# Kernel optimization log

Hardware: AMD Instinct MI355X
Metric: run time of the kernel (lower is better)

The kernel has to match this reference:

```python
import jax, jax.numpy as jnp
import numpy as np

H, E, K = 1024, 8, 2  # hidden_size, num_experts, top_k
B, S = 2, 4096


def setup_inputs() -> dict:
    key = jax.random.key(0)
    ks = jax.random.split(key, 5)
    s = 1.0 / np.sqrt(H)
    return {
        "x": jax.random.normal(ks[0], (B, S, H), dtype=jnp.float32),
        "ln_scale": jnp.ones((H,), jnp.float32),
        "ln_bias": jnp.zeros((H,), jnp.float32),
        "w1": (jax.random.normal(ks[1], (H, H), jnp.float32) * s),
        "b1": jnp.zeros((H,), jnp.float32),
        "w2": (jax.random.normal(ks[2], (H, E), jnp.float32) * s),
        "b2": jnp.zeros((E,), jnp.float32),
        "We": (jax.random.normal(ks[3], (E, H, H), jnp.float32) * s),
        "be": jnp.zeros((E, H), jnp.float32),
    }


def _layernorm(x, scale, bias, eps=1e-5):
    m = jnp.mean(x, axis=-1, keepdims=True)
    v = jnp.var(x, axis=-1, keepdims=True)
    return (x - m) * jax.lax.rsqrt(v + eps) * scale + bias


def reference(x, ln_scale, ln_bias, w1, b1, w2, b2, We, be):
    b, s, h = x.shape
    # --- router (BaseRouter): LN -> MLP -> softmax -> top-k -> renorm ---
    xn = _layernorm(x, ln_scale, ln_bias)
    hmid = jax.nn.relu(xn @ w1 + b1)
    logits = hmid @ w2 + b2                      # [B,S,E]
    probs = jax.nn.softmax(logits, axis=-1)
    topk_p, topk_i = jax.lax.top_k(probs, K)     # [B,S,K]
    topk_p = topk_p / jnp.sum(topk_p, axis=-1, keepdims=True)
    # sparse combine weights [B,S,E]: renormalized top-k gate, 0 elsewhere
    cw = jnp.sum(topk_p[..., None] * jax.nn.one_hot(topk_i, E, dtype=x.dtype), axis=-2)
    # --- expert dispatch / weighted combine ---
    t = b * s
    xf = x.reshape(t, h)
    cwf = cw.reshape(t, E)
    ye = jnp.einsum('th,ehd->etd', xf, We) + be[:, None, :]   # [E,T,H]
    out = jnp.einsum('te,etd->td', cwf, ye).reshape(b, s, h)
    # --- aux load-balance loss ---
    mean_p = jnp.mean(probs, axis=(0, 1))        # [E]
    aux = jnp.sum(mean_p * jnp.log(mean_p * E + 1e-9))
    return out, aux
```

## Files before the change

### kernel.cpp

```cpp
#include <hip/hip_runtime.h>
#include <hip/hip_fp16.h>

#define H 1024
#define E 8
#define TT 8192

typedef __attribute__((ext_vector_type(8))) short bf16x8;
typedef __attribute__((ext_vector_type(4))) float f32x4;

__device__ __forceinline__ unsigned short f2bf(float f) {
  unsigned int u = __float_as_uint(f);
  u += 0x7fffu + ((u >> 16) & 1u);
  return (unsigned short)(u >> 16);
}

__device__ __forceinline__ int swz(int row, int c) {
  return (row << 5) | (((c ^ (row >> 1)) & 3) << 3);
}

__device__ __forceinline__ void gld16(void* lds, const void* g) {
  __builtin_amdgcn_global_load_lds((const __attribute__((address_space(1))) void*)g,
                                   (__attribute__((address_space(3))) void*)lds, 16, 0, 0);
}

__global__ __launch_bounds__(64) void k_init(int* cnt, double* psum) {
  int t = threadIdx.x;
  if (t < E) { cnt[t] = 0; psum[t] = 0.0; }
}

__global__ __launch_bounds__(256) void k_cast_we(const float* __restrict__ we, unsigned short* __restrict__ wet) {
  __shared__ unsigned short tile[32][33];
  int e = blockIdx.z;
  int kb = blockIdx.x << 5, nb = blockIdx.y << 5;
  int t = threadIdx.x;
  int cc = t & 31, rr = t >> 5;
  size_t base = (size_t)e * H * H;
#pragma unroll
  for (int r = 0; r < 4; ++r) {
    int k = kb + rr + (r << 3);
    tile[rr + (r << 3)][cc] = f2bf(we[base + (size_t)k * H + nb + cc]);
  }
  __syncthreads();
#pragma unroll
  for (int r = 0; r < 4; ++r) {
    int n = nb + rr + (r << 3);
    wet[base + (size_t)n * H + kb + cc] = tile[cc][rr + (r << 3)];
  }
}

__global__ __launch_bounds__(256) void k_cast_w1(const float* __restrict__ w1, const float* __restrict__ lsc,
                                                 unsigned short* __restrict__ w1h, unsigned short* __restrict__ w1l) {
  __shared__ float tile[32][33];
  int kb = blockIdx.x << 5, nb = blockIdx.y << 5;
  int t = threadIdx.x;
  int cc = t & 31, rr = t >> 5;
#pragma unroll
  for (int r = 0; r < 4; ++r) {
    int k = kb + rr + (r << 3);
    tile[rr + (r << 3)][cc] = w1[(size_t)k * H + nb + cc] * lsc[k];
  }
  __syncthreads();
#pragma unroll
  for (int r = 0; r < 4; ++r) {
    int n = nb + rr + (r << 3);
    float v = tile[cc][rr + (r << 3)];
    unsigned short h = f2bf(v);
    float hv = __uint_as_float((unsigned)h << 16);
    unsigned short l = f2bf(v - hv);
    w1h[(size_t)n * H + kb + cc] = h;
    w1l[(size_t)n * H + kb + cc] = l;
  }
}

__global__ __launch_bounds__(256) void k_b1a(const float* __restrict__ w1, const float* __restrict__ lbi,
                                             float* __restrict__ part) {
  int bk = blockIdx.x, t = threadIdx.x;
  float a0 = 0, a1 = 0, a2 = 0, a3 = 0;
  for (int kk = 0; kk < 16; ++kk) {
    int k = (bk << 4) + kk;
    float lb = lbi[k];
    const float* row = &w1[(size_t)k * H];
    a0 = fmaf(lb, row[t], a0);
    a1 = fmaf(lb, row[t + 256], a1);
    a2 = fmaf(lb, row[t + 512], a2);
    a3 = fmaf(lb, row[t + 768], a3);
  }
  part[bk * H + t] = a0;
  part[bk * H + t + 256] = a1;
  part[bk * H + t + 512] = a2;
  part[bk * H + t + 768] = a3;
}

__global__ __launch_bounds__(256) void k_b1b(const float* __restrict__ part, const float* __restrict__ b1,
                                             float* __restrict__ b1eff) {
  int n = (blockIdx.x << 8) + threadIdx.x;
  float s = b1[n];
  for (int j = 0; j < 64; ++j) s += part[j * H + n];
  b1eff[n] = s;
}

__global__ __launch_bounds__(256) void k_stats(const float* __restrict__ x, float2* __restrict__ stats,
                                               unsigned short* __restrict__ xb) {
  int tok = blockIdx.x, t = threadIdx.x;
  const float4 v = *reinterpret_cast<const float4*>(&x[(size_t)tok * H + (t << 2)]);
  float s = v.x + v.y + v.z + v.w;
  float ss = v.x * v.x + v.y * v.y + v.z * v.z + v.w * v.w;
#pragma unroll
  for (int off = 32; off; off >>= 1) { s += __shfl_down(s, off); ss += __shfl_down(ss, off); }
  __shared__ float red[4][2];
  int lane = t & 63, wv = t >> 6;
  if (lane == 0) { red[wv][0] = s; red[wv][1] = ss; }
  __syncthreads();
  float fs = red[0][0] + red[1][0] + red[2][0] + red[3][0];
  float fss = red[0][1] + red[1][1] + red[2][1] + red[3][1];
  float mean = fs * (1.0f / H);
  float var = fss * (1.0f / H) - mean * mean;
  float rstd = rsqrtf(var + 1e-5f);
  if (t == 0) stats[tok] = make_float2(mean, rstd);
  ushort4 ob;
  ob.x = f2bf(v.x); ob.y = f2bf(v.y); ob.z = f2bf(v.z); ob.w = f2bf(v.w);
  *reinterpret_cast<ushort4*>(&xb[(size_t)tok * H + (t << 2)]) = ob;
}

__global__ __launch_bounds__(256) void k_router_mfma(
    const float* __restrict__ x, const float2* __restrict__ stats,
    const unsigned short* __restrict__ w1h, const unsigned short* __restrict__ w1l,
    const float* __restrict__ b1eff, const float* __restrict__ w2, float* __restrict__ plog) {
  __shared__ __align__(16) short At[2][8192];
  __shared__ __align__(16) short Bt[2][8192];
  int t = threadIdx.x;
  int d = blockIdx.x + (blockIdx.y << 6);
  int l = ((d & 7) << 6) + (d >> 3);
  int bm = (l & 63) << 7, bnb = l >> 6, bn = bnb << 7;
  int w = t >> 6, lane = t & 63;
  int s0 = (w << 8) + lane;
  int r0_ = s0 >> 2, cg0 = (s0 & 3) ^ ((r0_ >> 1) & 3);
  int s1 = s0 + 64, r1_ = s1 >> 2, cg1 = (s1 & 3) ^ ((r1_ >> 1) & 3);
  int s2 = s0 + 128, r2_ = s2 >> 2, cg2 = (s2 & 3) ^ ((r2_ >> 1) & 3);
  int s3 = s0 + 192, r3_ = s3 >> 2, cg3 = (s3 & 3) ^ ((r3_ >> 1) & 3);
  const unsigned short* srcB0 =
      ((r0_ < 128) ? &w1h[(size_t)(bn + r0_) * H] : &w1l[(size_t)(bn + r0_ - 128) * H]) + (cg0 << 3);
  const unsigned short* srcB1 =
      ((r1_ < 128) ? &w1h[(size_t)(bn + r1_) * H] : &w1l[(size_t)(bn + r1_ - 128) * H]) + (cg1 << 3);
  const unsigned short* srcB2 =
      ((r2_ < 128) ? &w1h[(size_t)(bn + r2_) * H] : &w1l[(size_t)(bn + r2_ - 128) * H]) + (cg2 << 3);
  const unsigned short* srcB3 =
      ((r3_ < 128) ? &w1h[(size_t)(bn + r3_) * H] : &w1l[(size_t)(bn + r3_ - 128) * H]) + (cg3 << 3);
  int dB0 = (w << 11), dB1 = dB0 + 512, dB2 = dB0 + 1024, dB3 = dB0 + 1536;
  int arow = t >> 1, ac0 = (t & 1) << 1;
  float2 mr = stats[bm + arow];
  float rsc = mr.y, mb = -mr.x * mr.y;
  const float* xsrc = &x[(size_t)(bm + arow) * H + (ac0 << 3)];
  int wA0 = swz(arow, ac0), wA1 = swz(arow, ac0 + 1);
  int wL0 = swz(arow + 128, ac0), wL1 = swz(arow + 128, ac0 + 1);
  float4 va0, va1, va2, va3;
  auto ldx = [&](int ko) {
    va0 = *(const float4*)(xsrc + ko + 0); va1 = *(const float4*)(xsrc + ko + 4);
    va2 = *(const float4*)(xsrc + ko + 8); va3 = *(const float4*)(xsrc + ko + 12);
  };
  auto stageB = [&](int b, int ko) {
    gld16(&Bt[b][dB0], srcB0 + ko); gld16(&Bt[b][dB1], srcB1 + ko);
    gld16(&Bt[b][dB2], srcB2 + ko); gld16(&Bt[b][dB3], srcB3 + ko);
  };
  auto split_store = [&](int b) {
    float zz[16];
    zz[0] = fmaf(va0.x, rsc, mb); zz[1] = fmaf(va0.y, rsc, mb);
    zz[2] = fmaf(va0.z, rsc, mb); zz[3] = fmaf(va0.w, rsc, mb);
    zz[4] = fmaf(va1.x, rsc, mb); zz[5] = fmaf(va1.y, rsc, mb);
    zz[6] = fmaf(va1.z, rsc, mb); zz[7] = fmaf(va1.w, rsc, mb);
    zz[8] = fmaf(va2.x, rsc, mb); zz[9] = fmaf(va2.y, rsc, mb);
    zz[10] = fmaf(va2.z, rsc, mb); zz[11] = fmaf(va2.w, rsc, mb);
    zz[12] = fmaf(va3.x, rsc, mb); zz[13] = fmaf(va3.y, rsc, mb);
    zz[14] = fmaf(va3.z, rsc, mb); zz[15] = fmaf(va3.w, rsc, mb);
    unsigned hw[8], lw[8];
#pragma unroll
    for (int p = 0; p < 8; ++p) {
      unsigned ua = __float_as_uint(zz[2 * p]), ub = __float_as_uint(zz[2 * p + 1]);
      hw[p] = (ua >> 16) | (ub & 0xffff0000u);
      float la = zz[2 * p] - __uint_as_float(ua & 0xffff0000u);
      float lb = zz[2 * p + 1] - __uint_as_float(ub & 0xffff0000u);
      lw[p] = (__float_as_uint(la) >> 16) | (__float_as_uint(lb) & 0xffff0000u);
    }
    *(int4*)&At[b][wA0] = make_int4(hw[0], hw[1], hw[2], hw[3]);
    *(int4*)&At[b][wA1] = make_int4(hw[4], hw[5], hw[6], hw[7]);
    *(int4*)&At[b][wL0] = make_int4(lw[0], lw[1], lw[2], lw[3]);
    *(int4*)&At[b][wL1] = make_int4(lw[4], lw[5], lw[6], lw[7]);
  };
  int wr = (w >> 1) << 6, wc = (w & 1) << 6;
  int l15 = lane & 15, lgp = lane >> 4;
  f32x4 acc[4][4];
#pragma unroll
  for (int i = 0; i < 4; ++i)
#pragma unroll
    for (int j = 0; j < 4; ++j) acc[i][j] = f32x4{0.f, 0.f, 0.f, 0.f};
  ldx(0);
  stageB(0, 0);
  split_store(0);
  for (int kt = 0; kt < 32; ++kt) {
    int b = kt & 1;
    if (kt < 31) {
      ldx((kt + 1) << 5);
      stageB(b ^ 1, (kt + 1) << 5);
    }
    if (kt < 31) {
      asm volatile("s_waitcnt vmcnt(8) lgkmcnt(0)" ::: "memory");
    } else {
      asm volatile("s_waitcnt vmcnt(0) lgkmcnt(0)" ::: "memory");
    }
    __builtin_amdgcn_s_barrier();
    bf16x8 bh[4], bl[4];
#pragma unroll
    for (int j = 0; j < 4; ++j) {
      bh[j] = *(const bf16x8*)&Bt[b][swz(wc + (j << 4) + l15, lgp)];
      bl[j] = *(const bf16x8*)&Bt[b][swz(128 + wc + (j << 4) + l15, lgp)];
    }
#pragma unroll
    for (int i = 0; i < 4; ++i) {
      bf16x8 ah = *(const bf16x8*)&At[b][swz(wr + (i << 4) + l15, lgp)];
      bf16x8 al = *(const bf16x8*)&At[b][swz(128 + wr + (i << 4) + l15, lgp)];
#pragma unroll
      for (int j = 0; j < 4; ++j) {
        acc[i][j] = __builtin_amdgcn_mfma_f32_16x16x32_bf16(ah, bh[j], acc[i][j], 0, 0, 0);
        acc[i][j] = __builtin_amdgcn_mfma_f32_16x16x32_bf16(ah, bl[j], acc[i][j], 0, 0, 0);
        acc[i][j] = __builtin_amdgcn_mfma_f32_16x16x32_bf16(al, bh[j], acc[i][j], 0, 0, 0);
      }
    }
    if (kt < 31) {
      split_store(b ^ 1);
      asm volatile("s_waitcnt lgkmcnt(0)" ::: "memory");
      __builtin_amdgcn_s_barrier();
    }
  }
  float w2r[4][8], b1r[4];
#pragma unroll
  for (int j = 0; j < 4; ++j) {
    int col = bn + wc + (j << 4) + l15;
    float4 p0 = *(const float4*)&w2[(size_t)col * E];
    float4 p1 = *(const float4*)&w2[(size_t)col * E + 4];
    w2r[j][0] = p0.x; w2r[j][1] = p0.y; w2r[j][2] = p0.z; w2r[j][3] = p0.w;
    w2r[j][4] = p1.x; w2r[j][5] = p1.y; w2r[j][6] = p1.z; w2r[j][7] = p1.w;
    b1r[j] = b1eff[col];
  }
#pragma unroll
  for (int i = 0; i < 4; ++i)
#pragma unroll
    for (int j = 0; j < 4; ++j)
#pragma unroll
      for (int r = 0; r < 4; ++r) acc[i][j][r] = fmaxf(acc[i][j][r] + b1r[j], 0.f);
  int wh = wc >> 6;
  size_t pbase = ((size_t)(bnb * 2 + wh) * TT + bm) * E;
#pragma unroll
  for (int e = 0; e < E; ++e) {
    float se[4][4];
#pragma unroll
    for (int i = 0; i < 4; ++i)
#pragma unroll
      for (int r = 0; r < 4; ++r)
        se[i][r] = acc[i][0][r] * w2r[0][e] + acc[i][1][r] * w2r[1][e] +
                   acc[i][2][r] * w2r[2][e] + acc[i][3][r] * w2r[3][e];
#pragma unroll
    for (int off = 1; off < 16; off <<= 1)
#pragma unroll
      for (int i = 0; i < 4; ++i)
#pragma unroll
        for (int r = 0; r < 4; ++r) se[i][r] += __shfl_xor(se[i][r], off);
    if (l15 == 0) {
#pragma unroll
      for (int i = 0; i < 4; ++i)
#pragma unroll
        for (int r = 0; r < 4; ++r) {
          int row = wr + (i << 4) + (lgp << 2) + r;
          plog[pbase + (size_t)row * E + e] = se[i][r];
        }
    }
  }
}

__global__ __launch_bounds__(256) void k_top(const float* __restrict__ plog, const float* __restrict__ b2,
                                             int* __restrict__ topE, float* __restrict__ topW,
                                             int* __restrict__ listIdx, float* __restrict__ listW,
                                             int* __restrict__ cnt, double* __restrict__ psum) {
  int t = threadIdx.x, lane = t & 63;
  int tok = (blockIdx.x << 8) + t;
  float lg[E], p[E];
  float4 ba = *reinterpret_cast<const float4*>(b2);
  float4 bb = *reinterpret_cast<const float4*>(b2 + 4);
  lg[0] = ba.x; lg[1] = ba.y; lg[2] = ba.z; lg[3] = ba.w;
  lg[4] = bb.x; lg[5] = bb.y; lg[6] = bb.z; lg[7] = bb.w;
#pragma unroll
  for (int nb = 0; nb < 16; ++nb) {
    const float* pp = &plog[((size_t)nb * TT + tok) * E];
    float4 q0 = *reinterpret_cast<const float4*>(pp);
    float4 q1 = *reinterpret_cast<const float4*>(pp + 4);
    lg[0] += q0.x; lg[1] += q0.y; lg[2] += q0.z; lg[3] += q0.w;
    lg[4] += q1.x; lg[5] += q1.y; lg[6] += q1.z; lg[7] += q1.w;
  }
  float m = lg[0];
#pragma unroll
  for (int e = 1; e < E; ++e) m = fmaxf(m, lg[e]);
  float s = 0.f;
#pragma unroll
  for (int e = 0; e < E; ++e) { p[e] = __expf(lg[e] - m); s += p[e]; }
  float inv = 1.f / s;
#pragma unroll
  for (int e = 0; e < E; ++e) p[e] *= inv;
  {
    float ps[E];
#pragma unroll
    for (int e = 0; e < E; ++e) ps[e] = p[e];
#pragma unroll
    for (int off = 1; off < 64; off <<= 1)
#pragma unroll
      for (int e = 0; e < E; ++e) ps[e] += __shfl_xor(ps[e], off);
    if (lane == 0)
#pragma unroll
      for (int e = 0; e < E; ++e) atomicAdd(&psum[e], (double)ps[e]);
  }
  int e0 = 0;
#pragma unroll
  for (int e = 1; e < E; ++e) if (p[e] > p[e0]) e0 = e;
  int e1 = (e0 == 0) ? 1 : 0;
#pragma unroll
  for (int e = 0; e < E; ++e) if (e != e0 && p[e] > p[e1]) e1 = e;
  float rsw = 1.f / (p[e0] + p[e1]);
  float w0 = p[e0] * rsw, w1v = p[e1] * rsw;
  topE[tok << 1] = e0; topE[(tok << 1) + 1] = e1;
  topW[tok << 1] = w0; topW[(tok << 1) + 1] = w1v;
  unsigned long long lt = (1ull << lane) - 1ull;
#pragma unroll
  for (int e = 0; e < E; ++e) {
    unsigned long long m0 = __ballot(e0 == e);
    unsigned long long m1 = __ballot(e1 == e);
    int n0 = __popcll(m0), total = n0 + __popcll(m1);
    if (total == 0) continue;
    int leader = __ffsll(m0 | m1) - 1;
    int base = 0;
    if (lane == leader) base = atomicAdd(&cnt[e], total);
    base = __shfl(base, leader);
    if (e0 == e) {
      int pos = e * TT + base + __popcll(m0 & lt);
      listIdx[pos] = (tok << 1); listW[pos] = w0;
    }
    if (e1 == e) {
      int pos = e * TT + base + n0 + __popcll(m1 & lt);
      listIdx[pos] = (tok << 1) | 1; listW[pos] = w1v;
    }
  }
}

__global__ __launch_bounds__(256) void k_expert_gemm(const unsigned short* __restrict__ xb,
                                                     const unsigned short* __restrict__ wet,
                                                     const int* __restrict__ listIdx, const float* __restrict__ listW,
                                                     const int* __restrict__ cnt, unsigned short* __restrict__ ys) {
  int d = blockIdx.x + (blockIdx.y << 6) + (blockIdx.z << 9);
  int l = ((d & 7) << 9) + (d >> 3);
  int e = l >> 9, by = (l >> 6) & 7, bx = l & 63;
  int c = cnt[e];
  int r0 = bx << 7;
  if (r0 >= c) return;
  int n0 = by << 7;
  __shared__ __align__(16) short A[3][4096], B[3][4096];
  __shared__ int gi[128];
  __shared__ float gw[128];
  int t = threadIdx.x;
  if (t < 128) {
    int rr = r0 + t;
    gi[t] = (rr < c) ? listIdx[e * TT + rr] : -1;
    gw[t] = (rr < c) ? listW[e * TT + rr] : 0.f;
  }
  __syncthreads();
  int w = t >> 6, lane = t & 63;
  int s0 = (w << 7) + lane, s1 = s0 + 64;
  int rA0 = s0 >> 2, cg0 = (s0 & 3) ^ ((rA0 >> 1) & 3);
  int rA1 = s1 >> 2, cg1 = (s1 & 3) ^ ((rA1 >> 1) & 3);
  int pk0 = gi[rA0], pk1 = gi[rA1];
  const unsigned short* srcA0 = &xb[(size_t)((pk0 < 0) ? 0 : (pk0 >> 1)) * H + (cg0 << 3)];
  const unsigned short* srcA1 = &xb[(size_t)((pk1 < 0) ? 0 : (pk1 >> 1)) * H + (cg1 << 3)];
  size_t wbase = (size_t)e * H * H;
  const unsigned short* srcB0 = &wet[wbase + (size_t)(n0 + rA0) * H + (cg0 << 3)];
  const unsigned short* srcB1 = &wet[wbase + (size_t)(n0 + rA1) * H + (cg1 << 3)];
  int d0 = (w << 10), d1 = d0 + 512;
  int wr = (w >> 1) << 6, wc = (w & 1) << 6;
  int l15 = lane & 15, lgp = lane >> 4;
  f32x4 acc[4][4];
#pragma unroll
  for (int i = 0; i < 4; ++i)
#pragma unroll
    for (int j = 0; j < 4; ++j) acc[i][j] = f32x4{0.f, 0.f, 0.f, 0.f};
#pragma unroll
  for (int pt = 0; pt < 3; ++pt) {
    int ko = pt << 5;
    gld16(&A[pt][d0], srcA0 + ko); gld16(&A[pt][d1], srcA1 + ko);
    gld16(&B[pt][d0], srcB0 + ko); gld16(&B[pt][d1], srcB1 + ko);
  }
  int b = 0;
  for (int kt = 0; kt < 32; ++kt) {
    if (kt <= 29) {
      asm volatile("s_waitcnt vmcnt(8)" ::: "memory");
    } else if (kt == 30) {
      asm volatile("s_waitcnt vmcnt(4)" ::: "memory");
    } else {
      asm volatile("s_waitcnt vmcnt(0)" ::: "memory");
    }
    __builtin_amdgcn_s_barrier();
    bf16x8 bq[4];
#pragma unroll
    for (int j = 0; j < 4; ++j) bq[j] = *(const bf16x8*)&B[b][swz(wc + (j << 4) + l15, lgp)];
#pragma unroll
    for (int i = 0; i < 4; ++i) {
      bf16x8 af = *(const bf16x8*)&A[b][swz(wr + (i << 4) + l15, lgp)];
#pragma unroll
      for (int j = 0; j < 4; ++j)
        acc[i][j] = __builtin_amdgcn_mfma_f32_16x16x32_bf16(af, bq[j], acc[i][j], 0, 0, 0);
    }
    if (kt < 29) {
      __builtin_amdgcn_s_barrier();
      int ko = (kt + 3) << 5;
      gld16(&A[b][d0], srcA0 + ko); gld16(&A[b][d1], srcA1 + ko);
      gld16(&B[b][d0], srcB0 + ko); gld16(&B[b][d1], srcB1 + ko);
    }
    b = (b == 2) ? 0 : b + 1;
  }
#pragma unroll
  for (int i = 0; i < 4; ++i) {
#pragma unroll
    for (int r = 0; r < 4; ++r) {
      int row = wr + (i << 4) + (lgp << 2) + r;
      int pk = gi[row];
      if (pk < 0) continue;
      int tok = pk >> 1, slot = pk & 1;
      float wgt = gw[row];
      size_t ob = ((size_t)slot * TT + tok) * H + n0 + wc + l15;
#pragma unroll
      for (int j = 0; j < 4; ++j) ys[ob + (j << 4)] = __half_as_ushort(__float2half(wgt * acc[i][j][r]));
    }
  }
}

__global__ __launch_bounds__(256) void k_combine(const unsigned short* __restrict__ ys, const int* __restrict__ topE,
                                                 const float* __restrict__ topW, const float* __restrict__ be,
                                                 float* __restrict__ out) {
  int tok = blockIdx.x, t = threadIdx.x;
  int e0 = topE[tok << 1], e1 = topE[(tok << 1) + 1];
  float w0 = topW[tok << 1], w1v = topW[(tok << 1) + 1];
  int h = t << 2;
  size_t base = (size_t)tok * H + h;
  ushort4 a = *reinterpret_cast<const ushort4*>(&ys[base]);
  ushort4 b = *reinterpret_cast<const ushort4*>(&ys[(size_t)TT * H + base]);
  float4 b0 = *reinterpret_cast<const float4*>(&be[e0 * H + h]);
  float4 b1v = *reinterpret_cast<const float4*>(&be[e1 * H + h]);
  float4 o;
  o.x = __half2float(__ushort_as_half(a.x)) + __half2float(__ushort_as_half(b.x)) + w0 * b0.x + w1v * b1v.x;
  o.y = __half2float(__ushort_as_half(a.y)) + __half2float(__ushort_as_half(b.y)) + w0 * b0.y + w1v * b1v.y;
  o.z = __half2float(__ushort_as_half(a.z)) + __half2float(__ushort_as_half(b.z)) + w0 * b0.z + w1v * b1v.z;
  o.w = __half2float(__ushort_as_half(a.w)) + __half2float(__ushort_as_half(b.w)) + w0 * b0.w + w1v * b1v.w;
  *reinterpret_cast<float4*>(&out[base]) = o;
}

__global__ __launch_bounds__(64) void k_aux(const double* __restrict__ psum, float* __restrict__ outAux) {
  if (threadIdx.x == 0) {
    double a = 0.0;
    for (int e = 0; e < E; ++e) {
      double mp = psum[e] / (double)TT;
      a += mp * log(mp * (double)E + 1e-9);
    }
    outAux[0] = (float)a;
  }
}

extern "C" void kernel_launch(void* const* d_in, const int* in_sizes, int n_in, void* d_out, int out_size, void* d_ws,
                              size_t ws_size, hipStream_t stream) {
  const float* x = (const float*)d_in[0];
  const float* lsc = (const float*)d_in[1];
  const float* lbi = (const float*)d_in[2];
  const float* w1 = (const float*)d_in[3];
  const float* b1 = (const float*)d_in[4];
  const float* w2 = (const float*)d_in[5];
  const float* b2 = (const float*)d_in[6];
  const float* we = (const float*)d_in[7];
  const float* be = (const float*)d_in[8];
  float* out = (float*)d_out;
  char* ws = (char*)d_ws;

  char* p = ws;
  float2* stats = (float2*)p; p += TT * 8;
  int* topE = (int*)p; p += TT * 2 * 4;
  float* topW = (float*)p; p += TT * 2 * 4;
  int* listIdx = (int*)p; p += E * TT * 4;
  float* listW = (float*)p; p += E * TT * 4;
  int* cnt = (int*)p; p += 256;
  double* psum = (double*)p; p += 2048;
  float* b1eff = (float*)p; p += H * 4;
  float* part = (float*)p; p += 64 * H * 4;
  unsigned short* xb = (unsigned short*)(ws + (2u << 20));
  unsigned short* wet = (unsigned short*)(ws + (18u << 20));
  unsigned short* w1h = (unsigned short*)(ws + (34u << 20));
  unsigned short* w1l = (unsigned short*)(ws + (36u << 20));
  float* plog = (float*)(ws + (38u << 20));
  unsigned short* ys = (unsigned short*)(ws + (34u << 20));

  k_init<<<1, 64, 0, stream>>>(cnt, psum);
  k_cast_w1<<<dim3(32, 32), 256, 0, stream>>>(w1, lsc, w1h, w1l);
  k_b1a<<<64, 256, 0, stream>>>(w1, lbi, part);
  k_b1b<<<4, 256, 0, stream>>>(part, b1, b1eff);
  k_cast_we<<<dim3(32, 32, E), 256, 0, stream>>>(we, wet);
  k_stats<<<TT, 256, 0, stream>>>(x, stats, xb);
  k_router_mfma<<<dim3(TT / 128, H / 128), 256, 0, stream>>>(x, stats, w1h, w1l, b1eff, w2, plog);
  k_top<<<TT / 256, 256, 0, stream>>>(plog, b2, topE, topW, listIdx, listW, cnt, psum);
  k_expert_gemm<<<dim3(TT / 128, H / 128, E), 256, 0, stream>>>(xb, wet, listIdx, listW, cnt, ys);
  k_combine<<<TT, 256, 0, stream>>>(ys, topE, topW, be, out);
  k_aux<<<1, 64, 0, stream>>>(psum, out + (size_t)TT * H);
}
```

Baseline: 250.5 us.

## Precompute split LN activations and load GEMM A-operands directly into registers

k_stats now writes the normalized activations as hi/lo bf16 arrays, so the router GEMM no longer reloads fp32 x and does the LN and split inside its K loop. Both the router and expert GEMMs now read their A fragments straight from global memory into registers with double buffering, and only B goes through a 3-stage LDS ring, which removes the A staging in LDS and one barrier per iteration. The grids are flattened to 1D with a remapped tile order, and the workspace is relaid so the expert-weight cast runs after the router. The cost is 32 MB of extra zh/zl global traffic and uncoalesced per-lane A loads, some of them gathered rows, that go straight to registers.

```diff
diff --git a/kernel.cpp b/kernel.cpp
--- a/kernel.cpp
+++ b/kernel.cpp
@@ -99,8 +99,8 @@
   b1eff[n] = s;
 }
 
-__global__ __launch_bounds__(256) void k_stats(const float* __restrict__ x, float2* __restrict__ stats,
-                                               unsigned short* __restrict__ xb) {
+__global__ __launch_bounds__(256) void k_stats(const float* __restrict__ x, unsigned short* __restrict__ xb,
+                                               unsigned short* __restrict__ zh, unsigned short* __restrict__ zl) {
   int tok = blockIdx.x, t = threadIdx.x;
   const float4 v = *reinterpret_cast<const float4*>(&x[(size_t)tok * H + (t << 2)]);
   float s = v.x + v.y + v.z + v.w;
@@ -116,119 +116,104 @@
   float mean = fs * (1.0f / H);
   float var = fss * (1.0f / H) - mean * mean;
   float rstd = rsqrtf(var + 1e-5f);
-  if (t == 0) stats[tok] = make_float2(mean, rstd);
+  float mb = -mean * rstd;
+  size_t base = (size_t)tok * H + (t << 2);
   ushort4 ob;
   ob.x = f2bf(v.x); ob.y = f2bf(v.y); ob.z = f2bf(v.z); ob.w = f2bf(v.w);
-  *reinterpret_cast<ushort4*>(&xb[(size_t)tok * H + (t << 2)]) = ob;
+  *reinterpret_cast<ushort4*>(&xb[base]) = ob;
+  float zz[4];
+  zz[0] = fmaf(v.x, rstd, mb); zz[1] = fmaf(v.y, rstd, mb);
+  zz[2] = fmaf(v.z, rstd, mb); zz[3] = fmaf(v.w, rstd, mb);
+  ushort4 oh, ol;
+  unsigned u0 = __float_as_uint(zz[0]), u1 = __float_as_uint(zz[1]);
+  unsigned u2 = __float_as_uint(zz[2]), u3 = __float_as_uint(zz[3]);
+  oh.x = (unsigned short)(u0 >> 16); oh.y = (unsigned short)(u1 >> 16);
+  oh.z = (unsigned short)(u2 >> 16); oh.w = (unsigned short)(u3 >> 16);
+  float l0 = zz[0] - __uint_as_float(u0 & 0xffff0000u);
+  float l1 = zz[1] - __uint_as_float(u1 & 0xffff0000u);
+  float l2 = zz[2] - __uint_as_float(u2 & 0xffff0000u);
+  float l3 = zz[3] - __uint_as_float(u3 & 0xffff0000u);
+  ol.x = (unsigned short)(__float_as_uint(l0) >> 16); ol.y = (unsigned short)(__float_as_uint(l1) >> 16);
+  ol.z = (unsigned short)(__float_as_uint(l2) >> 16); ol.w = (unsigned short)(__float_as_uint(l3) >> 16);
+  *reinterpret_cast<ushort4*>(&zh[base]) = oh;
+  *reinterpret_cast<ushort4*>(&zl[base]) = ol;
 }
 
 __global__ __launch_bounds__(256) void k_router_mfma(
-    const float* __restrict__ x, const float2* __restrict__ stats,
-    const unsigned short* __restrict__ w1h, const unsigned short* __restrict__ w1l,
+    const unsigned short* __restrict__ zh, const unsigned short* __restrict__ zl,
+    const unsigned short* __restrict__ w1h,
     const float* __restrict__ b1eff, const float* __restrict__ w2, float* __restrict__ plog) {
-  __shared__ __align__(16) short At[2][8192];
-  __shared__ __align__(16) short Bt[2][8192];
+  __shared__ __align__(16) short Bt[3][8192];
   int t = threadIdx.x;
-  int d = blockIdx.x + (blockIdx.y << 6);
+  int d = blockIdx.x;
   int l = ((d & 7) << 6) + (d >> 3);
-  int bm = (l & 63) << 7, bnb = l >> 6, bn = bnb << 7;
+  int bm = (l >> 3) << 7;
+  int bnb = l & 7, bn = bnb << 7;
   int w = t >> 6, lane = t & 63;
-  int s0 = (w << 8) + lane;
-  int r0_ = s0 >> 2, cg0 = (s0 & 3) ^ ((r0_ >> 1) & 3);
-  int s1 = s0 + 64, r1_ = s1 >> 2, cg1 = (s1 & 3) ^ ((r1_ >> 1) & 3);
-  int s2 = s0 + 128, r2_ = s2 >> 2, cg2 = (s2 & 3) ^ ((r2_ >> 1) & 3);
-  int s3 = s0 + 192, r3_ = s3 >> 2, cg3 = (s3 & 3) ^ ((r3_ >> 1) & 3);
-  const unsigned short* srcB0 =
-      ((r0_ < 128) ? &w1h[(size_t)(bn + r0_) * H] : &w1l[(size_t)(bn + r0_ - 128) * H]) + (cg0 << 3);
-  const unsigned short* srcB1 =
-      ((r1_ < 128) ? &w1h[(size_t)(bn + r1_) * H] : &w1l[(size_t)(bn + r1_ - 128) * H]) + (cg1 << 3);
-  const unsigned short* srcB2 =
-      ((r2_ < 128) ? &w1h[(size_t)(bn + r2_) * H] : &w1l[(size_t)(bn + r2_ - 128) * H]) + (cg2 << 3);
-  const unsigned short* srcB3 =
-      ((r3_ < 128) ? &w1h[(size_t)(bn + r3_) * H] : &w1l[(size_t)(bn + r3_ - 128) * H]) + (cg3 << 3);
-  int dB0 = (w << 11), dB1 = dB0 + 512, dB2 = dB0 + 1024, dB3 = dB0 + 1536;
-  int arow = t >> 1, ac0 = (t & 1) << 1;
-  float2 mr = stats[bm + arow];
-  float rsc = mr.y, mb = -mr.x * mr.y;
-  const float* xsrc = &x[(size_t)(bm + arow) * H + (ac0 << 3)];
-  int wA0 = swz(arow, ac0), wA1 = swz(arow, ac0 + 1);
-  int wL0 = swz(arow + 128, ac0), wL1 = swz(arow + 128, ac0 + 1);
-  float4 va0, va1, va2, va3;
-  auto ldx = [&](int ko) {
-    va0 = *(const float4*)(xsrc + ko + 0); va1 = *(const float4*)(xsrc + ko + 4);
-    va2 = *(const float4*)(xsrc + ko + 8); va3 = *(const float4*)(xsrc + ko + 12);
-  };
-  auto stageB = [&](int b, int ko) {
-    gld16(&Bt[b][dB0], srcB0 + ko); gld16(&Bt[b][dB1], srcB1 + ko);
-    gld16(&Bt[b][dB2], srcB2 + ko); gld16(&Bt[b][dB3], srcB3 + ko);
-  };
-  auto split_store = [&](int b) {
-    float zz[16];
-    zz[0] = fmaf(va0.x, rsc, mb); zz[1] = fmaf(va0.y, rsc, mb);
-    zz[2] = fmaf(va0.z, rsc, mb); zz[3] = fmaf(va0.w, rsc, mb);
-    zz[4] = fmaf(va1.x, rsc, mb); zz[5] = fmaf(va1.y, rsc, mb);
-    zz[6] = fmaf(va1.z, rsc, mb); zz[7] = fmaf(va1.w, rsc, mb);
-    zz[8] = fmaf(va2.x, rsc, mb); zz[9] = fmaf(va2.y, rsc, mb);
-    zz[10] = fmaf(va2.z, rsc, mb); zz[11] = fmaf(va2.w, rsc, mb);
-    zz[12] = fmaf(va3.x, rsc, mb); zz[13] = fmaf(va3.y, rsc, mb);
-    zz[14] = fmaf(va3.z, rsc, mb); zz[15] = fmaf(va3.w, rsc, mb);
-    unsigned hw[8], lw[8];
-#pragma unroll
-    for (int p = 0; p < 8; ++p) {
-      unsigned ua = __float_as_uint(zz[2 * p]), ub = __float_as_uint(zz[2 * p + 1]);
-      hw[p] = (ua >> 16) | (ub & 0xffff0000u);
-      float la = zz[2 * p] - __uint_as_float(ua & 0xffff0000u);
-      float lb = zz[2 * p + 1] - __uint_as_float(ub & 0xffff0000u);
-      lw[p] = (__float_as_uint(la) >> 16) | (__float_as_uint(lb) & 0xffff0000u);
-    }
-    *(int4*)&At[b][wA0] = make_int4(hw[0], hw[1], hw[2], hw[3]);
-    *(int4*)&At[b][wA1] = make_int4(hw[4], hw[5], hw[6], hw[7]);
-    *(int4*)&At[b][wL0] = make_int4(lw[0], lw[1], lw[2], lw[3]);
-    *(int4*)&At[b][wL1] = make_int4(lw[4], lw[5], lw[6], lw[7]);
-  };
+  int l15 = lane & 15, lgp = lane >> 4;
   int wr = (w >> 1) << 6, wc = (w & 1) << 6;
-  int l15 = lane & 15, lgp = lane >> 4;
+  int sl = (w << 8) + lane;
+  int bo[4];
+#pragma unroll
+  for (int q = 0; q < 4; ++q) {
+    int s = sl + (q << 6);
+    int r = s >> 2, cg = (s & 3) ^ ((r >> 1) & 3);
+    bo[q] = ((r < 128) ? (bn + r) * H : 1048576 + (bn + r - 128) * H) + (cg << 3);
+  }
+  int dB = w << 11;
+  int zo[4];
+#pragma unroll
+  for (int i = 0; i < 4; ++i) zo[i] = (bm + wr + (i << 4) + l15) * H + (lgp << 3);
   f32x4 acc[4][4];
 #pragma unroll
   for (int i = 0; i < 4; ++i)
 #pragma unroll
     for (int j = 0; j < 4; ++j) acc[i][j] = f32x4{0.f, 0.f, 0.f, 0.f};
-  ldx(0);
-  stageB(0, 0);
-  split_store(0);
+  bf16x8 ah[2][4], al[2][4];
+#pragma unroll
+  for (int q = 0; q < 4; ++q) gld16(&Bt[0][dB + (q << 9)], w1h + bo[q]);
+#pragma unroll
+  for (int q = 0; q < 4; ++q) gld16(&Bt[1][dB + (q << 9)], w1h + bo[q] + 32);
+#pragma unroll
+  for (int i = 0; i < 4; ++i) {
+    ah[0][i] = *(const bf16x8*)(zh + zo[i]);
+    al[0][i] = *(const bf16x8*)(zl + zo[i]);
+  }
+#pragma unroll
   for (int kt = 0; kt < 32; ++kt) {
-    int b = kt & 1;
+    const int cur = kt & 1, nxt = cur ^ 1;
     if (kt < 31) {
-      ldx((kt + 1) << 5);
-      stageB(b ^ 1, (kt + 1) << 5);
-    }
-    if (kt < 31) {
-      asm volatile("s_waitcnt vmcnt(8) lgkmcnt(0)" ::: "memory");
+      const int ko = (kt + 1) << 5;
+#pragma unroll
+      for (int i = 0; i < 4; ++i) {
+        ah[nxt][i] = *(const bf16x8*)(zh + zo[i] + ko);
+        al[nxt][i] = *(const bf16x8*)(zl + zo[i] + ko);
+      }
+    }
+    if (kt <= 30) {
+      asm volatile("s_waitcnt vmcnt(12)" ::: "memory");
     } else {
-      asm volatile("s_waitcnt vmcnt(0) lgkmcnt(0)" ::: "memory");
-    }
+      asm volatile("s_waitcnt vmcnt(0)" ::: "memory");
+    }
+    __builtin_amdgcn_sched_barrier(0);
     __builtin_amdgcn_s_barrier();
-    bf16x8 bh[4], bl[4];
+    __builtin_amdgcn_sched_barrier(0);
+    if (kt < 30) {
+      const int bnxt = (kt + 2) % 3, ko = (kt + 2) << 5;
+#pragma unroll
+      for (int q = 0; q < 4; ++q) gld16(&Bt[bnxt][dB + (q << 9)], w1h + bo[q] + ko);
+    }
+    const int bb = kt % 3;
 #pragma unroll
     for (int j = 0; j < 4; ++j) {
-      bh[j] = *(const bf16x8*)&Bt[b][swz(wc + (j << 4) + l15, lgp)];
-      bl[j] = *(const bf16x8*)&Bt[b][swz(128 + wc + (j << 4) + l15, lgp)];
-    }
-#pragma unroll
-    for (int i = 0; i < 4; ++i) {
-      bf16x8 ah = *(const bf16x8*)&At[b][swz(wr + (i << 4) + l15, lgp)];
-      bf16x8 al = *(const bf16x8*)&At[b][swz(128 + wr + (i << 4) + l15, lgp)];
-#pragma unroll
-      for (int j = 0; j < 4; ++j) {
-        acc[i][j] = __builtin_amdgcn_mfma_f32_16x16x32_bf16(ah, bh[j], acc[i][j], 0, 0, 0);
-        acc[i][j] = __builtin_amdgcn_mfma_f32_16x16x32_bf16(ah, bl[j], acc[i][j], 0, 0, 0);
-        acc[i][j] = __builtin_amdgcn_mfma_f32_16x16x32_bf16(al, bh[j], acc[i][j], 0, 0, 0);
+      bf16x8 bh = *(const bf16x8*)&Bt[bb][swz(wc + (j << 4) + l15, lgp)];
+      bf16x8 bl = *(const bf16x8*)&Bt[bb][swz(128 + wc + (j << 4) + l15, lgp)];
+#pragma unroll
+      for (int i = 0; i < 4; ++i) {
+        acc[i][j] = __builtin_amdgcn_mfma_f32_16x16x32_bf16(ah[cur][i], bh, acc[i][j], 0, 0, 0);
+        acc[i][j] = __builtin_amdgcn_mfma_f32_16x16x32_bf16(ah[cur][i], bl, acc[i][j], 0, 0, 0);
+        acc[i][j] = __builtin_amdgcn_mfma_f32_16x16x32_bf16(al[cur][i], bh, acc[i][j], 0, 0, 0);
       }
-    }
-    if (kt < 31) {
-      split_store(b ^ 1);
-      asm volatile("s_waitcnt lgkmcnt(0)" ::: "memory");
-      __builtin_amdgcn_s_barrier();
     }
   }
   float w2r[4][8], b1r[4];
@@ -352,14 +337,16 @@
                                                      const unsigned short* __restrict__ wet,
                                                      const int* __restrict__ listIdx, const float* __restrict__ listW,
                                                      const int* __restrict__ cnt, unsigned short* __restrict__ ys) {
-  int d = blockIdx.x + (blockIdx.y << 6) + (blockIdx.z << 9);
+  int d = blockIdx.x;
   int l = ((d & 7) << 9) + (d >> 3);
-  int e = l >> 9, by = (l >> 6) & 7, bx = l & 63;
+  int e = l >> 9;
+  int lx = l & 511;
+  int bx = lx >> 3, by = lx & 7;
   int c = cnt[e];
   int r0 = bx << 7;
   if (r0 >= c) return;
   int n0 = by << 7;
-  __shared__ __align__(16) short A[3][4096], B[3][4096];
+  __shared__ __align__(16) short B[3][4096];
   __shared__ int gi[128];
   __shared__ float gw[128];
   int t = threadIdx.x;
@@ -370,56 +357,66 @@
   }
   __syncthreads();
   int w = t >> 6, lane = t & 63;
-  int s0 = (w << 7) + lane, s1 = s0 + 64;
-  int rA0 = s0 >> 2, cg0 = (s0 & 3) ^ ((rA0 >> 1) & 3);
-  int rA1 = s1 >> 2, cg1 = (s1 & 3) ^ ((rA1 >> 1) & 3);
-  int pk0 = gi[rA0], pk1 = gi[rA1];
-  const unsigned short* srcA0 = &xb[(size_t)((pk0 < 0) ? 0 : (pk0 >> 1)) * H + (cg0 << 3)];
-  const unsigned short* srcA1 = &xb[(size_t)((pk1 < 0) ? 0 : (pk1 >> 1)) * H + (cg1 << 3)];
-  size_t wbase = (size_t)e * H * H;
-  const unsigned short* srcB0 = &wet[wbase + (size_t)(n0 + rA0) * H + (cg0 << 3)];
-  const unsigned short* srcB1 = &wet[wbase + (size_t)(n0 + rA1) * H + (cg1 << 3)];
-  int d0 = (w << 10), d1 = d0 + 512;
+  int l15 = lane & 15, lgp = lane >> 4;
   int wr = (w >> 1) << 6, wc = (w & 1) << 6;
-  int l15 = lane & 15, lgp = lane >> 4;
+  int sl = (w << 7) + lane;
+  int ebase = e << 20;
+  int bo[2];
+#pragma unroll
+  for (int q = 0; q < 2; ++q) {
+    int s = sl + (q << 6);
+    int r = s >> 2, cg = (s & 3) ^ ((r >> 1) & 3);
+    bo[q] = ebase + (n0 + r) * H + (cg << 3);
+  }
+  int dB = w << 10;
+  int ao[4];
+#pragma unroll
+  for (int i = 0; i < 4; ++i) {
+    int pk = gi[wr + (i << 4) + l15];
+    int tok = (pk < 0) ? 0 : (pk >> 1);
+    ao[i] = tok * H + (lgp << 3);
+  }
   f32x4 acc[4][4];
 #pragma unroll
   for (int i = 0; i < 4; ++i)
 #pragma unroll
     for (int j = 0; j < 4; ++j) acc[i][j] = f32x4{0.f, 0.f, 0.f, 0.f};
-#pragma unroll
-  for (int pt = 0; pt < 3; ++pt) {
-    int ko = pt << 5;
-    gld16(&A[pt][d0], srcA0 + ko); gld16(&A[pt][d1], srcA1 + ko);
-    gld16(&B[pt][d0], srcB0 + ko); gld16(&B[pt][d1], srcB1 + ko);
-  }
-  int b = 0;
+  bf16x8 a[2][4];
+#pragma unroll
+  for (int q = 0; q < 2; ++q) gld16(&B[0][dB + (q << 9)], wet + bo[q]);
+#pragma unroll
+  for (int q = 0; q < 2; ++q) gld16(&B[1][dB + (q << 9)], wet + bo[q] + 32);
+#pragma unroll
+  for (int i = 0; i < 4; ++i) a[0][i] = *(const bf16x8*)(xb + ao[i]);
+#pragma unroll
   for (int kt = 0; kt < 32; ++kt) {
-    if (kt <= 29) {
-      asm volatile("s_waitcnt vmcnt(8)" ::: "memory");
-    } else if (kt == 30) {
-      asm volatile("s_waitcnt vmcnt(4)" ::: "memory");
+    const int cur = kt & 1, nxt = cur ^ 1;
+    if (kt < 31) {
+      const int ko = (kt + 1) << 5;
+#pragma unroll
+      for (int i = 0; i < 4; ++i) a[nxt][i] = *(const bf16x8*)(xb + ao[i] + ko);
+    }
+    if (kt <= 30) {
+      asm volatile("s_waitcnt vmcnt(6)" ::: "memory");
     } else {
       asm volatile("s_waitcnt vmcnt(0)" ::: "memory");
     }
+    __builtin_amdgcn_sched_barrier(0);
     __builtin_amdgcn_s_barrier();
-    bf16x8 bq[4];
-#pragma unroll
-    for (int j = 0; j < 4; ++j) bq[j] = *(const bf16x8*)&B[b][swz(wc + (j << 4) + l15, lgp)];
-#pragma unroll
-    for (int i = 0; i < 4; ++i) {
-      bf16x8 af = *(const bf16x8*)&A[b][swz(wr + (i << 4) + l15, lgp)];
-#pragma unroll
-      for (int j = 0; j < 4; ++j)
-        acc[i][j] = __builtin_amdgcn_mfma_f32_16x16x32_bf16(af, bq[j], acc[i][j], 0, 0, 0);
-    }
-    if (kt < 29) {
-      __builtin_amdgcn_s_barrier();
-      int ko = (kt + 3) << 5;
-      gld16(&A[b][d0], srcA0 + ko); gld16(&A[b][d1], srcA1 + ko);
-      gld16(&B[b][d0], srcB0 + ko); gld16(&B[b][d1], srcB1 + ko);
-    }
-    b = (b == 2) ? 0 : b + 1;
+    __builtin_amdgcn_sched_barrier(0);
+    if (kt < 30) {
+      const int bnxt = (kt + 2) % 3, ko = (kt + 2) << 5;
+#pragma unroll
+      for (int q = 0; q < 2; ++q) gld16(&B[bnxt][dB + (q << 9)], wet + bo[q] + ko);
+    }
+    const int bb = kt % 3;
+#pragma unroll
+    for (int j = 0; j < 4; ++j) {
+      bf16x8 bq = *(const bf16x8*)&B[bb][swz(wc + (j << 4) + l15, lgp)];
+#pragma unroll
+      for (int i = 0; i < 4; ++i)
+        acc[i][j] = __builtin_amdgcn_mfma_f32_16x16x32_bf16(a[cur][i], bq, acc[i][j], 0, 0, 0);
+    }
   }
 #pragma unroll
   for (int i = 0; i < 4; ++i) {
@@ -483,7 +480,6 @@
   char* ws = (char*)d_ws;
 
   char* p = ws;
-  float2* stats = (float2*)p; p += TT * 8;
   int* topE = (int*)p; p += TT * 2 * 4;
   float* topW = (float*)p; p += TT * 2 * 4;
   int* listIdx = (int*)p; p += E * TT * 4;
@@ -492,22 +488,24 @@
   double* psum = (double*)p; p += 2048;
   float* b1eff = (float*)p; p += H * 4;
   float* part = (float*)p; p += 64 * H * 4;
-  unsigned short* xb = (unsigned short*)(ws + (2u << 20));
-  unsigned short* wet = (unsigned short*)(ws + (18u << 20));
-  unsigned short* w1h = (unsigned short*)(ws + (34u << 20));
-  unsigned short* w1l = (unsigned short*)(ws + (36u << 20));
-  float* plog = (float*)(ws + (38u << 20));
-  unsigned short* ys = (unsigned short*)(ws + (34u << 20));
+  unsigned short* xb = (unsigned short*)(ws + (2ull << 20));
+  unsigned short* zh = (unsigned short*)(ws + (18ull << 20));
+  unsigned short* zl = (unsigned short*)(ws + (34ull << 20));
+  unsigned short* w1h = (unsigned short*)(ws + (50ull << 20));
+  unsigned short* w1l = (unsigned short*)(ws + (52ull << 20));
+  float* plog = (float*)(ws + (54ull << 20));
+  unsigned short* wet = (unsigned short*)(ws + (18ull << 20));
+  unsigned short* ys = (unsigned short*)(ws + (34ull << 20));
 
   k_init<<<1, 64, 0, stream>>>(cnt, psum);
   k_cast_w1<<<dim3(32, 32), 256, 0, stream>>>(w1, lsc, w1h, w1l);
   k_b1a<<<64, 256, 0, stream>>>(w1, lbi, part);
   k_b1b<<<4, 256, 0, stream>>>(part, b1, b1eff);
+  k_stats<<<TT, 256, 0, stream>>>(x, xb, zh, zl);
+  k_router_mfma<<<512, 256, 0, stream>>>(zh, zl, w1h, b1eff, w2, plog);
+  k_top<<<TT / 256, 256, 0, stream>>>(plog, b2, topE, topW, listIdx, listW, cnt, psum);
   k_cast_we<<<dim3(32, 32, E), 256, 0, stream>>>(we, wet);
-  k_stats<<<TT, 256, 0, stream>>>(x, stats, xb);
-  k_router_mfma<<<dim3(TT / 128, H / 128), 256, 0, stream>>>(x, stats, w1h, w1l, b1eff, w2, plog);
-  k_top<<<TT / 256, 256, 0, stream>>>(plog, b2, topE, topW, listIdx, listW, cnt, psum);
-  k_expert_gemm<<<dim3(TT / 128, H / 128, E), 256, 0, stream>>>(xb, wet, listIdx, listW, cnt, ys);
+  k_expert_gemm<<<4096, 256, 0, stream>>>(xb, wet, listIdx, listW, cnt, ys);
   k_combine<<<TT, 256, 0, stream>>>(ys, topE, topW, be, out);
   k_aux<<<1, 64, 0, stream>>>(psum, out + (size_t)TT * H);
 }
```

Measured after the change: 315.7 us. +26.0%, slower.
